# Performance work log

Measured on AMD Instinct MI355X. Metric: run time of the kernel, lower is better.

## Reference

```python
import jax, jax.numpy as jnp
import numpy as np

DIM = 1024          # BIGNET_DIM
LORA = 32
GROUP = 128
N_LIN = 18          # 6 blocks * 3 QLoRALinear
N_LN = 5
EPS = 1e-5


def setup_inputs() -> dict:
    key = jax.random.key(0)
    ks = jax.random.split(key, 8)
    tokens = 16384
    x = jax.random.normal(ks[0], (tokens, DIM), dtype=jnp.float32)
    # int4 codes in [0,16), per-(out,group) scale (block-abs-max norm)
    q = jax.random.randint(ks[1], (N_LIN, DIM, DIM), 0, 16, dtype=jnp.int32)
    norm = jax.random.uniform(ks[2], (N_LIN, DIM, DIM // GROUP), dtype=jnp.float32) * 0.1 + 0.01
    bias = jax.random.normal(ks[3], (N_LIN, DIM), dtype=jnp.float32) * 0.01
    # lora_a: kaiming-uniform * 0.01; lora_b: zeros in the original init, but we use
    # small random values so the LoRA path (and its gradients) are exercised.
    lora_a = jax.random.normal(ks[4], (N_LIN, LORA, DIM), dtype=jnp.float32) * 0.01
    lora_b = jax.random.normal(ks[5], (N_LIN, DIM, LORA), dtype=jnp.float32) * 0.01
    ln_gamma = jnp.ones((N_LN, DIM), dtype=jnp.float32)
    ln_beta = jnp.zeros((N_LN, DIM), dtype=jnp.float32)
    return {"x": x, "q": q, "norm": norm, "bias": bias,
            "lora_a": lora_a, "lora_b": lora_b,
            "ln_gamma": ln_gamma, "ln_beta": ln_beta}


def _dequant(qi, ni):
    # qi: [O, I] int codes in [0,16); ni: [O, I//GROUP] group scales
    O, I = qi.shape
    w = (qi.astype(jnp.float32) / 15.0 * 2.0 - 1.0).reshape(O, I // GROUP, GROUP)
    return (w * ni[..., None]).reshape(O, I)


def _qlora_linear(h, qi, ni, b, la, lb):
    w = _dequant(qi, ni)                      # [O, I]
    base = h @ w.T + b                        # frozen quantized path
    lora = (h @ la.T) @ lb.T                  # rank-32 adapter
    return base + lora


def _layernorm(h, g, b):
    mu = jnp.mean(h, axis=-1, keepdims=True)
    var = jnp.var(h, axis=-1, keepdims=True)
    return (h - mu) * jax.lax.rsqrt(var + EPS) * g + b


def _forward(x, q, norm, bias, lora_a, lora_b, ln_gamma, ln_beta):
    h = x
    for blk in range(6):
        r = h
        for j in range(3):
            i = 3 * blk + j
            r = _qlora_linear(r, q[i], norm[i], bias[i], lora_a[i], lora_b[i])
            if j < 2:
                r = jax.nn.relu(r)
        h = r + h                              # residual
        if blk < 5:
            h = _layernorm(h, ln_gamma[blk], ln_beta[blk])
    return h


def reference(x, q, norm, bias, lora_a, lora_b, ln_gamma, ln_beta):
    return _forward(x, q, norm, bias, lora_a, lora_b, ln_gamma, ln_beta)
```

## Files before the change

kernel.cpp:

```cpp
#include <hip/hip_runtime.h>
#include <stdint.h>


#define TOK   16384
#define DIM   1024
#define NLIN  18
#define EPS   1e-5f

typedef _Float16 f16;
typedef _Float16 f16x8 __attribute__((ext_vector_type(8)));
typedef _Float16 f16x4 __attribute__((ext_vector_type(4)));
typedef float    f32x4 __attribute__((ext_vector_type(4)));

__device__ __forceinline__ void load_lds16(const void* g, void* l) {
  __builtin_amdgcn_global_load_lds(
      (const __attribute__((address_space(1))) void*)g,
      (__attribute__((address_space(3))) void*)l,
      16, 0, 0);
}

__global__ __launch_bounds__(256) void prep_w2(
    const int* __restrict__ q, const float* __restrict__ norm,
    const float* __restrict__ la, const float* __restrict__ lb,
    f16* __restrict__ W)
{
  __shared__ float lbs[128 * 32];
  const int bid   = blockIdx.x;
  const int i     = bid >> 5;
  const int ot    = (bid >> 2) & 7;
  const int ktile = bid & 3;
  const int o0 = ot * 128, k0 = ktile * 256;
  const int tid = threadIdx.x;
  const int kg = tid & 63, og = tid >> 6;
  const int k4 = k0 + kg * 4;

  const float* lbsrc = lb + (size_t)i * DIM * 32 + (size_t)o0 * 32;
  #pragma unroll
  for (int p = 0; p < 4; ++p)
    *(float4*)(lbs + p * 1024 + tid * 4) = *(const float4*)(lbsrc + p * 1024 + tid * 4);

  float4 lar[32];
  const float* lasrc = la + (size_t)i * 32 * DIM + k4;
  #pragma unroll
  for (int r = 0; r < 32; ++r) lar[r] = *(const float4*)(lasrc + r * DIM);
  __syncthreads();

  const float s = 2.f / 15.f;
  for (int oi = 0; oi < 32; ++oi) {
    const int o = o0 + og * 32 + oi;
    const size_t wb = ((size_t)i * DIM + o) * DIM;
    const int4 qv = *(const int4*)(q + wb + k4);
    const float nrm = norm[((size_t)i * DIM + o) * 8 + (k4 >> 7)];
    const float* lbr = lbs + (og * 32 + oi) * 32;
    float ax = 0.f, ay = 0.f, az = 0.f, aw = 0.f;
    #pragma unroll
    for (int r = 0; r < 32; ++r) {
      const float b = lbr[r];
      ax += b * lar[r].x; ay += b * lar[r].y; az += b * lar[r].z; aw += b * lar[r].w;
    }
    f16x4 hv;
    hv[0] = (f16)(((float)qv.x * s - 1.f) * nrm + ax);
    hv[1] = (f16)(((float)qv.y * s - 1.f) * nrm + ay);
    hv[2] = (f16)(((float)qv.z * s - 1.f) * nrm + az);
    hv[3] = (f16)(((float)qv.w * s - 1.f) * nrm + aw);
    *(f16x4*)(W + wb + k4) = hv;
  }
}

__global__ __launch_bounds__(256) void cvt_x(
    const float* __restrict__ x, f16* __restrict__ o)
{
  const size_t idx = ((size_t)blockIdx.x * 256 + threadIdx.x) * 4;
  const float4 v = *(const float4*)(x + idx);
  f16x4 h;
  h[0] = (f16)v.x; h[1] = (f16)v.y; h[2] = (f16)v.z; h[3] = (f16)v.w;
  *(f16x4*)(o + idx) = h;
}

template<int EPI>
__global__ __launch_bounds__(512, 2) void gemm2(
    const f16* __restrict__ A, const f16* __restrict__ W,
    const float* __restrict__ bias, const f16* __restrict__ resid,
    void* __restrict__ outp)
{
  __shared__ __align__(16) char smem[131072];

  const int orig = blockIdx.x;
  const int swzb = (orig & 7) * 32 + (orig >> 3);
  const int mt = swzb >> 2, nt = swzb & 3;
  const int t0 = mt * 256, n0 = nt * 256;

  const int tid  = threadIdx.x;
  const int lane = tid & 63;
  const int wid  = tid >> 6;
  const int wm = wid >> 2, wn = wid & 3;

  const int srow   = tid >> 2;
  const int schunk = (tid & 3) ^ ((tid >> 3) & 3);
  const f16* gA = A + (size_t)(t0 + srow) * DIM + schunk * 8;
  const f16* gB = W + (size_t)(n0 + srow) * DIM + schunk * 8;
  const int sdst = tid * 16;

  const int kchunk = ((lane >> 4) ^ ((lane >> 1) & 3)) * 16;
  int aoff[8], boff[4];
  #pragma unroll
  for (int mi = 0; mi < 8; ++mi)
    aoff[mi] = (wm * 128 + mi * 16 + (lane & 15)) * 64 + kchunk;
  #pragma unroll
  for (int ni = 0; ni < 4; ++ni)
    boff[ni] = 16384 + (wn * 64 + ni * 16 + (lane & 15)) * 64 + kchunk;

  f32x4 acc[8][4] = {};

  auto stage = [&](int kt, int b) {
    const f16* as = gA + kt * 32;
    const f16* bs = gB + kt * 32;
    char* d = smem + b * 32768 + sdst;
    load_lds16(as, d);
    load_lds16(as + (size_t)128 * DIM, d + 8192);
    load_lds16(bs, d + 16384);
    load_lds16(bs + (size_t)128 * DIM, d + 24576);
  };
  auto body = [&](int b) {
    const char* base = smem + b * 32768;
    f16x8 af[8], bf[4];
    #pragma unroll
    for (int ni = 0; ni < 4; ++ni) bf[ni] = *(const f16x8*)(base + boff[ni]);
    #pragma unroll
    for (int mi = 0; mi < 8; ++mi) af[mi] = *(const f16x8*)(base + aoff[mi]);
    __builtin_amdgcn_s_setprio(1);
    #pragma unroll
    for (int mi = 0; mi < 8; ++mi)
      #pragma unroll
      for (int ni = 0; ni < 4; ++ni)
        acc[mi][ni] = __builtin_amdgcn_mfma_f32_16x16x32_f16(
            af[mi], bf[ni], acc[mi][ni], 0, 0, 0);
    __builtin_amdgcn_s_setprio(0);
  };

  stage(0, 0); stage(1, 1); stage(2, 2);

  for (int t = 0; t < 30; ++t) {
    asm volatile("s_waitcnt vmcnt(8)" ::: "memory");
    __builtin_amdgcn_s_barrier();
    __builtin_amdgcn_sched_barrier(0);
    if (t < 29) stage(t + 3, (t + 3) & 3);
    body(t & 3);
  }
  asm volatile("s_waitcnt vmcnt(4)" ::: "memory");
  __builtin_amdgcn_s_barrier();
  __builtin_amdgcn_sched_barrier(0);
  body(2);
  asm volatile("s_waitcnt vmcnt(0)" ::: "memory");
  __builtin_amdgcn_s_barrier();
  __builtin_amdgcn_sched_barrier(0);
  body(3);

  const int colb = lane & 15;
  const int rowb = (lane >> 4) << 2;
  #pragma unroll
  for (int ni = 0; ni < 4; ++ni) {
    const int col = n0 + wn * 64 + ni * 16 + colb;
    const float bv = bias[col];
    #pragma unroll
    for (int mi = 0; mi < 8; ++mi) {
      const int trow = t0 + wm * 128 + mi * 16 + rowb;
      const f32x4 v = acc[mi][ni];
      #pragma unroll
      for (int r = 0; r < 4; ++r) {
        const size_t idx = (size_t)(trow + r) * DIM + col;
        float val = v[r] + bv;
        if constexpr (EPI == 0) {
          val = fmaxf(val, 0.f);
          ((f16*)outp)[idx] = (f16)val;
        } else if constexpr (EPI == 1) {
          val += (float)resid[idx];
          ((f16*)outp)[idx] = (f16)val;
        } else {
          val += (float)resid[idx];
          ((float*)outp)[idx] = val;
        }
      }
    }
  }
}

__global__ __launch_bounds__(256) void ln_k(
    const f16* __restrict__ in, f16* __restrict__ out,
    const float* __restrict__ g, const float* __restrict__ b)
{
  __shared__ float red[8];
  const int row = blockIdx.x;
  const int tid = threadIdx.x;
  const int c = tid * 4;
  const f16x4 v4 = *(const f16x4*)(in + (size_t)row * DIM + c);
  const float v0 = v4[0], v1 = v4[1], v2 = v4[2], v3 = v4[3];
  float s  = v0 + v1 + v2 + v3;
  float s2 = v0 * v0 + v1 * v1 + v2 * v2 + v3 * v3;
  #pragma unroll
  for (int off = 32; off; off >>= 1) {
    s  += __shfl_xor(s,  off);
    s2 += __shfl_xor(s2, off);
  }
  if ((tid & 63) == 0) { red[(tid >> 6) * 2] = s; red[(tid >> 6) * 2 + 1] = s2; }
  __syncthreads();
  s  = red[0] + red[2] + red[4] + red[6];
  s2 = red[1] + red[3] + red[5] + red[7];
  const float mu  = s * (1.f / DIM);
  const float var = fmaxf(s2 * (1.f / DIM) - mu * mu, 0.f);
  const float rs  = rsqrtf(var + EPS);
  const float4 gv = *(const float4*)(g + c);
  const float4 bv = *(const float4*)(b + c);
  f16x4 o4;
  o4[0] = (f16)((v0 - mu) * rs * gv.x + bv.x);
  o4[1] = (f16)((v1 - mu) * rs * gv.y + bv.y);
  o4[2] = (f16)((v2 - mu) * rs * gv.z + bv.z);
  o4[3] = (f16)((v3 - mu) * rs * gv.w + bv.w);
  *(f16x4*)(out + (size_t)row * DIM + c) = o4;
}

extern "C" void kernel_launch(void* const* d_in, const int* in_sizes, int n_in,
                              void* d_out, int out_size, void* d_ws, size_t ws_size,
                              hipStream_t stream)
{
  (void)in_sizes; (void)n_in; (void)out_size; (void)ws_size;
  const float* x     = (const float*)d_in[0];
  const int*   q     = (const int*)d_in[1];
  const float* norm  = (const float*)d_in[2];
  const float* bias  = (const float*)d_in[3];
  const float* la    = (const float*)d_in[4];
  const float* lb    = (const float*)d_in[5];
  const float* lg    = (const float*)d_in[6];
  const float* lbeta = (const float*)d_in[7];

  char* ws = (char*)d_ws;
  f16* W    = (f16*)ws;
  f16* buf1 = (f16*)(ws + (size_t)NLIN * DIM * DIM * 2);
  f16* buf2 = buf1 + (size_t)TOK * DIM;
  f16* buf0 = (f16*)d_out;
  f16* bufs[3] = {buf0, buf1, buf2};

  prep_w2<<<NLIN * 32, 256, 0, stream>>>(q, norm, la, lb, W);
  cvt_x<<<TOK * DIM / 1024, 256, 0, stream>>>(x, buf0);

  int h = 0;
  for (int blk = 0; blk < 6; ++blk) {
    const int a = (h == 0) ? 1 : 0;
    const int p = 3 - h - a;
    const int i0 = blk * 3;
    const size_t wsz = (size_t)DIM * DIM;
    gemm2<0><<<256, 512, 0, stream>>>(bufs[h], W + (i0 + 0) * wsz,
                                      bias + (i0 + 0) * DIM, nullptr, bufs[a]);
    gemm2<0><<<256, 512, 0, stream>>>(bufs[a], W + (i0 + 1) * wsz,
                                      bias + (i0 + 1) * DIM, nullptr, bufs[p]);
    if (blk < 5) {
      gemm2<1><<<256, 512, 0, stream>>>(bufs[p], W + (i0 + 2) * wsz,
                                        bias + (i0 + 2) * DIM, bufs[h], bufs[a]);
      ln_k<<<TOK, 256, 0, stream>>>(bufs[a], bufs[a], lg + blk * DIM, lbeta + blk * DIM);
      h = a;
    } else {
      gemm2<2><<<256, 512, 0, stream>>>(bufs[p], W + (i0 + 2) * wsz,
                                        bias + (i0 + 2) * DIM, bufs[h], d_out);
    }
  }
}
```

Before: 1.045 ms.

## Restructure GEMM main loop to 64-wide K tiles with double buffering and split phases

The GEMM main loop moves from a 4-stage ring of 32-wide K tiles to two buffers of 64-wide K tiles (16 iterations), using a new XOR swizzle for the 128-byte rows. Each iteration is split into four phases, each reading fragments from LDS and issuing half of the MFMAs, with the next tile's global-to-LDS loads interleaved between phases. The aim is to halve the per-K-step barrier overhead and overlap LDS reads with MFMA work. In exchange it adds many more barriers per iteration, keeps only one tile of global prefetch in flight, and waits on vmcnt(0) every iteration, which may expose memory latency.

```diff
diff --git a/kernel.cpp b/kernel.cpp
--- a/kernel.cpp
+++ b/kernel.cpp
@@ -77,8 +77,48 @@
   *(f16x4*)(o + idx) = h;
 }
 
+#define BARX()   __builtin_amdgcn_s_barrier()
+#define LGKM0()  do { asm volatile("s_waitcnt lgkmcnt(0)" ::: "memory"); \
+                      __builtin_amdgcn_sched_barrier(0); } while (0)
+#define VMC0()   do { asm volatile("s_waitcnt vmcnt(0)" ::: "memory"); \
+                      __builtin_amdgcn_sched_barrier(0); } while (0)
+
+#define RD_AF(so, kk) do { \
+  _Pragma("unroll") \
+  for (int mi = 0; mi < 8; ++mi) \
+    af[mi] = *(const f16x8*)(smem + (so) + arowb[mi] + (ckA ^ ((kk) << 6))); \
+} while (0)
+
+#define RD_BF(so, ni0, kk) do { \
+  bf[ni0]     = *(const f16x8*)(smem + 65536 + (so) + browb[ni0]     + (ckA ^ ((kk) << 6))); \
+  bf[(ni0)+1] = *(const f16x8*)(smem + 65536 + (so) + browb[(ni0)+1] + (ckA ^ ((kk) << 6))); \
+} while (0)
+
+#define QUAD(ni0) do { \
+  __builtin_amdgcn_s_setprio(1); \
+  _Pragma("unroll") \
+  for (int mi = 0; mi < 8; ++mi) { \
+    acc[mi][ni0]     = __builtin_amdgcn_mfma_f32_16x16x32_f16(af[mi], bf[ni0],     acc[mi][ni0],     0, 0, 0); \
+    acc[mi][(ni0)+1] = __builtin_amdgcn_mfma_f32_16x16x32_f16(af[mi], bf[(ni0)+1], acc[mi][(ni0)+1], 0, 0, 0); \
+  } \
+  __builtin_amdgcn_s_setprio(0); \
+} while (0)
+
+#define STAGE_A(kt, dstso) do { \
+  _Pragma("unroll") \
+  for (int qq = 0; qq < 4; ++qq) \
+    load_lds16(gA + (size_t)(kt) * 64 + (size_t)qq * 64 * DIM, \
+               smem + (dstso) + qq * 8192 + sdst); \
+} while (0)
+#define STAGE_B(kt, dstso) do { \
+  _Pragma("unroll") \
+  for (int qq = 0; qq < 4; ++qq) \
+    load_lds16(gB + (size_t)(kt) * 64 + (size_t)qq * 64 * DIM, \
+               smem + 65536 + (dstso) + qq * 8192 + sdst); \
+} while (0)
+
 template<int EPI>
-__global__ __launch_bounds__(512, 2) void gemm2(
+__global__ __launch_bounds__(512, 2) void gemm3(
     const f16* __restrict__ A, const f16* __restrict__ W,
     const float* __restrict__ bias, const f16* __restrict__ resid,
     void* __restrict__ outp)
@@ -95,66 +135,45 @@
   const int wid  = tid >> 6;
   const int wm = wid >> 2, wn = wid & 3;
 
-  const int srow   = tid >> 2;
-  const int schunk = (tid & 3) ^ ((tid >> 3) & 3);
-  const f16* gA = A + (size_t)(t0 + srow) * DIM + schunk * 8;
-  const f16* gB = W + (size_t)(n0 + srow) * DIM + schunk * 8;
+  const int srow = tid >> 3;
+  const int sch  = (tid & 7) ^ (srow & 7);
+  const f16* gA = A + (size_t)(t0 + srow) * DIM + sch * 8;
+  const f16* gB = W + (size_t)(n0 + srow) * DIM + sch * 8;
   const int sdst = tid * 16;
 
-  const int kchunk = ((lane >> 4) ^ ((lane >> 1) & 3)) * 16;
-  int aoff[8], boff[4];
+  const int ckA = (((lane >> 4) ^ (lane & 7)) << 4);
+  int arowb[8], browb[4];
   #pragma unroll
   for (int mi = 0; mi < 8; ++mi)
-    aoff[mi] = (wm * 128 + mi * 16 + (lane & 15)) * 64 + kchunk;
+    arowb[mi] = (wm * 128 + mi * 16 + (lane & 15)) * 128;
   #pragma unroll
   for (int ni = 0; ni < 4; ++ni)
-    boff[ni] = 16384 + (wn * 64 + ni * 16 + (lane & 15)) * 64 + kchunk;
+    browb[ni] = (wn * 64 + ni * 16 + (lane & 15)) * 128;
 
   f32x4 acc[8][4] = {};
-
-  auto stage = [&](int kt, int b) {
-    const f16* as = gA + kt * 32;
-    const f16* bs = gB + kt * 32;
-    char* d = smem + b * 32768 + sdst;
-    load_lds16(as, d);
-    load_lds16(as + (size_t)128 * DIM, d + 8192);
-    load_lds16(bs, d + 16384);
-    load_lds16(bs + (size_t)128 * DIM, d + 24576);
-  };
-  auto body = [&](int b) {
-    const char* base = smem + b * 32768;
-    f16x8 af[8], bf[4];
-    #pragma unroll
-    for (int ni = 0; ni < 4; ++ni) bf[ni] = *(const f16x8*)(base + boff[ni]);
-    #pragma unroll
-    for (int mi = 0; mi < 8; ++mi) af[mi] = *(const f16x8*)(base + aoff[mi]);
-    __builtin_amdgcn_s_setprio(1);
-    #pragma unroll
-    for (int mi = 0; mi < 8; ++mi)
-      #pragma unroll
-      for (int ni = 0; ni < 4; ++ni)
-        acc[mi][ni] = __builtin_amdgcn_mfma_f32_16x16x32_f16(
-            af[mi], bf[ni], acc[mi][ni], 0, 0, 0);
-    __builtin_amdgcn_s_setprio(0);
-  };
-
-  stage(0, 0); stage(1, 1); stage(2, 2);
-
-  for (int t = 0; t < 30; ++t) {
-    asm volatile("s_waitcnt vmcnt(8)" ::: "memory");
-    __builtin_amdgcn_s_barrier();
-    __builtin_amdgcn_sched_barrier(0);
-    if (t < 29) stage(t + 3, (t + 3) & 3);
-    body(t & 3);
-  }
-  asm volatile("s_waitcnt vmcnt(4)" ::: "memory");
-  __builtin_amdgcn_s_barrier();
-  __builtin_amdgcn_sched_barrier(0);
-  body(2);
-  asm volatile("s_waitcnt vmcnt(0)" ::: "memory");
-  __builtin_amdgcn_s_barrier();
-  __builtin_amdgcn_sched_barrier(0);
-  body(3);
+  f16x8 af[8], bf[4];
+
+  STAGE_A(0, 0);
+  STAGE_B(0, 0);
+  VMC0();
+  BARX();
+
+  for (int t = 0; t < 16; ++t) {
+    const int so = (t & 1) << 15;
+    const int od = ((t + 1) & 1) << 15;
+    const bool st = (t < 15);
+    RD_AF(so, 0); RD_BF(so, 0, 0);
+    if (st) STAGE_A(t + 1, od);
+    BARX(); LGKM0(); QUAD(0); BARX();
+    RD_BF(so, 2, 0);
+    if (st) STAGE_B(t + 1, od);
+    BARX(); LGKM0(); QUAD(2); BARX();
+    RD_AF(so, 1); RD_BF(so, 0, 1);
+    BARX(); LGKM0(); QUAD(0); BARX();
+    RD_BF(so, 2, 1);
+    VMC0();
+    BARX(); LGKM0(); QUAD(2); BARX();
+  }
 
   const int colb = lane & 15;
   const int rowb = (lane >> 4) << 2;
@@ -249,17 +268,17 @@
     const int p = 3 - h - a;
     const int i0 = blk * 3;
     const size_t wsz = (size_t)DIM * DIM;
-    gemm2<0><<<256, 512, 0, stream>>>(bufs[h], W + (i0 + 0) * wsz,
+    gemm3<0><<<256, 512, 0, stream>>>(bufs[h], W + (i0 + 0) * wsz,
                                       bias + (i0 + 0) * DIM, nullptr, bufs[a]);
-    gemm2<0><<<256, 512, 0, stream>>>(bufs[a], W + (i0 + 1) * wsz,
+    gemm3<0><<<256, 512, 0, stream>>>(bufs[a], W + (i0 + 1) * wsz,
                                       bias + (i0 + 1) * DIM, nullptr, bufs[p]);
     if (blk < 5) {
-      gemm2<1><<<256, 512, 0, stream>>>(bufs[p], W + (i0 + 2) * wsz,
+      gemm3<1><<<256, 512, 0, stream>>>(bufs[p], W + (i0 + 2) * wsz,
                                         bias + (i0 + 2) * DIM, bufs[h], bufs[a]);
       ln_k<<<TOK, 256, 0, stream>>>(bufs[a], bufs[a], lg + blk * DIM, lbeta + blk * DIM);
       h = a;
     } else {
-      gemm2<2><<<256, 512, 0, stream>>>(bufs[p], W + (i0 + 2) * wsz,
+      gemm3<2><<<256, 512, 0, stream>>>(bufs[p], W + (i0 + 2) * wsz,
                                         bias + (i0 + 2) * DIM, bufs[h], d_out);
     }
   }
```

New measurement: 1.036 ms. Within noise of the previous version (-0.9%).

## Switch GEMM to 128x128 tiles with 64-wide K steps and double buffering

Applied to the files above, without the earlier changes.

The GEMM kernel moves from 256x256 tiles with 512 threads and a 4-deep 32-wide K pipeline to 128x128 tiles with 256 threads, 64-wide K steps and two LDS buffers. The grid grows from 256 to 1024 blocks and LDS use drops to 64KB, so more blocks can be resident per CU and the 256 CUs get a more even load. Fragments are read into registers before the next stage is issued, with an added barrier, and the XOR swizzle is rewritten for the 128-byte rows. In exchange, the smaller tiles mean each element loaded from global memory is reused less.

```diff
diff --git a/kernel.cpp b/kernel.cpp
--- a/kernel.cpp
+++ b/kernel.cpp
@@ -77,84 +77,89 @@
   *(f16x4*)(o + idx) = h;
 }
 
+#define BARX() __builtin_amdgcn_s_barrier()
+
+#define LDA6(sb, mi, kk) (*(const f16x8*)(smem + (sb) + arowb[mi] + (ckA ^ ((kk) << 6))))
+#define LDB6(sb, ni, kk) (*(const f16x8*)(smem + (sb) + 16384 + browb[ni] + (ckA ^ ((kk) << 6))))
+
+#define STAGE_T(T, base) do { \
+  _Pragma("unroll") \
+  for (int g = 0; g < 4; ++g) \
+    load_lds16(gA + (size_t)((T) * 64) + (size_t)(g * 32) * DIM, \
+               smem + (base) + g * 4096 + sdst); \
+  _Pragma("unroll") \
+  for (int g = 0; g < 4; ++g) \
+    load_lds16(gB + (size_t)((T) * 64) + (size_t)(g * 32) * DIM, \
+               smem + (base) + 16384 + g * 4096 + sdst); \
+} while (0)
+
 template<int EPI>
-__global__ __launch_bounds__(512, 2) void gemm2(
+__global__ __launch_bounds__(256, 2) void gemm6(
     const f16* __restrict__ A, const f16* __restrict__ W,
     const float* __restrict__ bias, const f16* __restrict__ resid,
     void* __restrict__ outp)
 {
-  __shared__ __align__(16) char smem[131072];
+  __shared__ __align__(16) char smem[65536];
 
   const int orig = blockIdx.x;
-  const int swzb = (orig & 7) * 32 + (orig >> 3);
-  const int mt = swzb >> 2, nt = swzb & 3;
-  const int t0 = mt * 256, n0 = nt * 256;
+  const int swzb = (orig & 7) * 128 + (orig >> 3);
+  const int mt = swzb >> 3, nt = swzb & 7;
+  const int t0 = mt * 128, n0 = nt * 128;
 
   const int tid  = threadIdx.x;
   const int lane = tid & 63;
   const int wid  = tid >> 6;
-  const int wm = wid >> 2, wn = wid & 3;
-
-  const int srow   = tid >> 2;
-  const int schunk = (tid & 3) ^ ((tid >> 3) & 3);
-  const f16* gA = A + (size_t)(t0 + srow) * DIM + schunk * 8;
-  const f16* gB = W + (size_t)(n0 + srow) * DIM + schunk * 8;
+  const int wm = wid >> 1, wn = wid & 1;
+
+  const int srow = tid >> 3;
+  const int sch  = (tid & 7) ^ (srow & 7);
+  const f16* gA = A + (size_t)(t0 + srow) * DIM + sch * 8;
+  const f16* gB = W + (size_t)(n0 + srow) * DIM + sch * 8;
   const int sdst = tid * 16;
 
-  const int kchunk = ((lane >> 4) ^ ((lane >> 1) & 3)) * 16;
-  int aoff[8], boff[4];
-  #pragma unroll
-  for (int mi = 0; mi < 8; ++mi)
-    aoff[mi] = (wm * 128 + mi * 16 + (lane & 15)) * 64 + kchunk;
+  const int ckA = (((lane >> 4) ^ (lane & 7)) << 4);
+  int arowb[4], browb[4];
+  #pragma unroll
+  for (int mi = 0; mi < 4; ++mi)
+    arowb[mi] = (wm * 64 + mi * 16 + (lane & 15)) * 128;
   #pragma unroll
   for (int ni = 0; ni < 4; ++ni)
-    boff[ni] = 16384 + (wn * 64 + ni * 16 + (lane & 15)) * 64 + kchunk;
-
-  f32x4 acc[8][4] = {};
-
-  auto stage = [&](int kt, int b) {
-    const f16* as = gA + kt * 32;
-    const f16* bs = gB + kt * 32;
-    char* d = smem + b * 32768 + sdst;
-    load_lds16(as, d);
-    load_lds16(as + (size_t)128 * DIM, d + 8192);
-    load_lds16(bs, d + 16384);
-    load_lds16(bs + (size_t)128 * DIM, d + 24576);
-  };
-  auto body = [&](int b) {
-    const char* base = smem + b * 32768;
-    f16x8 af[8], bf[4];
-    #pragma unroll
-    for (int ni = 0; ni < 4; ++ni) bf[ni] = *(const f16x8*)(base + boff[ni]);
-    #pragma unroll
-    for (int mi = 0; mi < 8; ++mi) af[mi] = *(const f16x8*)(base + aoff[mi]);
+    browb[ni] = (wn * 64 + ni * 16 + (lane & 15)) * 128;
+
+  f32x4 acc[4][4] = {};
+  f16x8 af[4][2], bf[4][2];
+
+  STAGE_T(0, 0);
+  STAGE_T(1, 32768);
+
+  for (int t = 0; t < 16; ++t) {
+    const int so = (t & 1) << 15;
+    if (t < 15) asm volatile("s_waitcnt vmcnt(8)" ::: "memory");
+    else        asm volatile("s_waitcnt vmcnt(0)" ::: "memory");
+    BARX();
+    #pragma unroll
+    for (int mi = 0; mi < 4; ++mi) {
+      af[mi][0] = LDA6(so, mi, 0); af[mi][1] = LDA6(so, mi, 1);
+    }
+    #pragma unroll
+    for (int ni = 0; ni < 4; ++ni) {
+      bf[ni][0] = LDB6(so, ni, 0); bf[ni][1] = LDB6(so, ni, 1);
+    }
+    BARX();
+    if (t < 14) STAGE_T(t + 2, so);
+    __builtin_amdgcn_sched_barrier(0);
     __builtin_amdgcn_s_setprio(1);
     #pragma unroll
-    for (int mi = 0; mi < 8; ++mi)
+    for (int mi = 0; mi < 4; ++mi)
       #pragma unroll
-      for (int ni = 0; ni < 4; ++ni)
+      for (int ni = 0; ni < 4; ++ni) {
         acc[mi][ni] = __builtin_amdgcn_mfma_f32_16x16x32_f16(
-            af[mi], bf[ni], acc[mi][ni], 0, 0, 0);
+            af[mi][0], bf[ni][0], acc[mi][ni], 0, 0, 0);
+        acc[mi][ni] = __builtin_amdgcn_mfma_f32_16x16x32_f16(
+            af[mi][1], bf[ni][1], acc[mi][ni], 0, 0, 0);
+      }
     __builtin_amdgcn_s_setprio(0);
-  };
-
-  stage(0, 0); stage(1, 1); stage(2, 2);
-
-  for (int t = 0; t < 30; ++t) {
-    asm volatile("s_waitcnt vmcnt(8)" ::: "memory");
-    __builtin_amdgcn_s_barrier();
-    __builtin_amdgcn_sched_barrier(0);
-    if (t < 29) stage(t + 3, (t + 3) & 3);
-    body(t & 3);
-  }
-  asm volatile("s_waitcnt vmcnt(4)" ::: "memory");
-  __builtin_amdgcn_s_barrier();
-  __builtin_amdgcn_sched_barrier(0);
-  body(2);
-  asm volatile("s_waitcnt vmcnt(0)" ::: "memory");
-  __builtin_amdgcn_s_barrier();
-  __builtin_amdgcn_sched_barrier(0);
-  body(3);
+  }
 
   const int colb = lane & 15;
   const int rowb = (lane >> 4) << 2;
@@ -163,8 +168,8 @@
     const int col = n0 + wn * 64 + ni * 16 + colb;
     const float bv = bias[col];
     #pragma unroll
-    for (int mi = 0; mi < 8; ++mi) {
-      const int trow = t0 + wm * 128 + mi * 16 + rowb;
+    for (int mi = 0; mi < 4; ++mi) {
+      const int trow = t0 + wm * 64 + mi * 16 + rowb;
       const f32x4 v = acc[mi][ni];
       #pragma unroll
       for (int r = 0; r < 4; ++r) {
@@ -249,18 +254,18 @@
     const int p = 3 - h - a;
     const int i0 = blk * 3;
     const size_t wsz = (size_t)DIM * DIM;
-    gemm2<0><<<256, 512, 0, stream>>>(bufs[h], W + (i0 + 0) * wsz,
-                                      bias + (i0 + 0) * DIM, nullptr, bufs[a]);
-    gemm2<0><<<256, 512, 0, stream>>>(bufs[a], W + (i0 + 1) * wsz,
-                                      bias + (i0 + 1) * DIM, nullptr, bufs[p]);
+    gemm6<0><<<1024, 256, 0, stream>>>(bufs[h], W + (i0 + 0) * wsz,
+                                       bias + (i0 + 0) * DIM, nullptr, bufs[a]);
+    gemm6<0><<<1024, 256, 0, stream>>>(bufs[a], W + (i0 + 1) * wsz,
+                                       bias + (i0 + 1) * DIM, nullptr, bufs[p]);
     if (blk < 5) {
-      gemm2<1><<<256, 512, 0, stream>>>(bufs[p], W + (i0 + 2) * wsz,
-                                        bias + (i0 + 2) * DIM, bufs[h], bufs[a]);
+      gemm6<1><<<1024, 256, 0, stream>>>(bufs[p], W + (i0 + 2) * wsz,
+                                         bias + (i0 + 2) * DIM, bufs[h], bufs[a]);
       ln_k<<<TOK, 256, 0, stream>>>(bufs[a], bufs[a], lg + blk * DIM, lbeta + blk * DIM);
       h = a;
     } else {
-      gemm2<2><<<256, 512, 0, stream>>>(bufs[p], W + (i0 + 2) * wsz,
-                                        bias + (i0 + 2) * DIM, bufs[h], d_out);
-    }
-  }
-}
+      gemm6<2><<<1024, 256, 0, stream>>>(bufs[p], W + (i0 + 2) * wsz,
+                                         bias + (i0 + 2) * DIM, bufs[h], d_out);
+    }
+  }
+}
```

New measurement: 967.5 us. -7.4%, faster.
